# Kernel tuning notes

Hardware: AMD Instinct MI355X
Metric: run time of the kernel (lower is better)

Reference implementation:

```python
import jax, jax.numpy as jnp
import numpy as np


def setup_inputs() -> dict:
    key = jax.random.key(0)
    k1, k2 = jax.random.split(key)
    p_hat = jax.random.normal(k1, (16384, 3), dtype=jnp.float32)
    p = jax.random.normal(k2, (16384, 3), dtype=jnp.float32)
    return {"p_hat": p_hat, "p": p}


def reference(p_hat, p):
    # squared pairwise L2 distances: ||a-b||^2 = ||a||^2 + ||b||^2 - 2 a.b
    a2 = jnp.sum(p_hat * p_hat, axis=-1)            # [N]
    b2 = jnp.sum(p * p, axis=-1)                    # [M]
    cross = p_hat @ p.T                             # [N, M]
    d2 = jnp.maximum(a2[:, None] + b2[None, :] - 2.0 * cross, 0.0)
    # Chamfer: mean of col-mins (min over dim 0) + mean of row-mins (min over dim 1)
    return jnp.mean(jnp.min(d2, axis=0)) + jnp.mean(jnp.min(d2, axis=1))
```

## Files before the change

kernel.cpp:

```cpp
#include <hip/hip_runtime.h>
#include <hip/hip_bf16.h>

#define N 16384
#define TPB 256
#define QPT 4
#define QTILE (TPB * QPT)
#define NQT (N / QTILE)
#define SPLIT 64
#define CHUNK (N / SPLIT)
#define GRID (2 * SPLIT * NQT)
#define INF_BITS 0x7F800000

__global__ void pack_kernel(const float* __restrict__ p_hat,
                            const float* __restrict__ p,
                            float4* __restrict__ q4,
                            int* __restrict__ minbuf) {
    int idx = blockIdx.x * blockDim.x + threadIdx.x;
    if (idx >= 2 * N) return;
    const float* src = (idx < N) ? p_hat : p;
    int k = (idx < N) ? idx : idx - N;
    float x = src[3 * k + 0], y = src[3 * k + 1], z = src[3 * k + 2];
    q4[idx] = make_float4(x, y, z, x * x + y * y + z * z);
    minbuf[idx] = INF_BITS;
}

__global__ void __launch_bounds__(TPB) chamfer_kernel(const float4* __restrict__ q4,
                                                      int* __restrict__ minbuf) {
    int b    = blockIdx.x;
    int dir  = b & 1;
    int rest = b >> 1;
    int jc   = rest & (SPLIT - 1);
    int qt   = rest >> 6;

    const float4* __restrict__ qp = q4 + (dir ? N : 0);
    const float4* __restrict__ rp = q4 + (dir ? 0 : N);

    int ibase = qt * QTILE + (int)threadIdx.x;
    float m2x[QPT], m2y[QPT], m2z[QPT], qw[QPT], vmin[QPT];
#pragma unroll
    for (int q = 0; q < QPT; ++q) {
        float4 qq = qp[ibase + q * TPB];
        m2x[q] = -2.0f * qq.x; m2y[q] = -2.0f * qq.y; m2z[q] = -2.0f * qq.z;
        qw[q] = qq.w;
        vmin[q] = __builtin_inff();
    }

    int j0 = j0 = jc * CHUNK;
    float4 ra = rp[j0];
    float4 rb = rp[j0 + 1];
#pragma unroll 2
    for (int j = j0; j < j0 + CHUNK; j += 2) {
        float4 na = rp[j + 2];
        float4 nb = rp[j + 3];
        float raw = ra.w, rbw = rb.w;
#pragma unroll
        for (int q = 0; q < QPT; ++q) {
            float ta = __builtin_fmaf(ra.x, m2x[q],
                       __builtin_fmaf(ra.y, m2y[q],
                       __builtin_fmaf(ra.z, m2z[q], raw)));
            float tb = __builtin_fmaf(rb.x, m2x[q],
                       __builtin_fmaf(rb.y, m2y[q],
                       __builtin_fmaf(rb.z, m2z[q], rbw)));
            asm("v_min3_f32 %0, %0, %1, %2" : "+v"(vmin[q]) : "v"(ta), "v"(tb));
        }
        ra = na; rb = nb;
    }

#pragma unroll
    for (int q = 0; q < QPT; ++q) {
        float m = fmaxf(vmin[q] + qw[q], 0.0f);
        atomicMin(&minbuf[dir * N + ibase + q * TPB], __float_as_int(m));
    }
}

__global__ void __launch_bounds__(1024) reduce_kernel(const int* __restrict__ minbuf,
                                                      float* __restrict__ out) {
    const int4* mb4 = (const int4*)minbuf;
    float s = 0.0f;
#pragma unroll
    for (int k = 0; k < (2 * N / 4) / 1024; ++k) {
        int4 v = mb4[k * 1024 + threadIdx.x];
        s += __int_as_float(v.x) + __int_as_float(v.y) +
             __int_as_float(v.z) + __int_as_float(v.w);
    }
    for (int off = 32; off > 0; off >>= 1) s += __shfl_down(s, off, 64);
    __shared__ float partial[1024 / 64];
    int lane = threadIdx.x & 63;
    int wid  = threadIdx.x >> 6;
    if (lane == 0) partial[wid] = s;
    __syncthreads();
    if (threadIdx.x == 0) {
        float t = 0.0f;
        for (int w = 0; w < 1024 / 64; ++w) t += partial[w];
        out[0] = t / (float)N;
    }
}

extern "C" void kernel_launch(void* const* d_in, const int* in_sizes, int n_in,
                              void* d_out, int out_size, void* d_ws, size_t ws_size,
                              hipStream_t stream) {
    const float* p_hat = (const float*)d_in[0];
    const float* p     = (const float*)d_in[1];
    float4* q4     = (float4*)d_ws;
    int*    minbuf = (int*)((char*)d_ws + 2 * N * sizeof(float4));
    float*  out    = (float*)d_out;

    pack_kernel<<<(2 * N + TPB - 1) / TPB, TPB, 0, stream>>>(p_hat, p, q4, minbuf);
    chamfer_kernel<<<GRID, TPB, 0, stream>>>(q4, minbuf);
    reduce_kernel<<<1, 1024, 0, stream>>>(minbuf, out);
}
```

Baseline: 109.5 us.

## Compute pairwise distances with bf16 split-precision MFMA and fused row/col mins

Replaces the scalar FMA distance loop with 16x16x32 bf16 MFMA tiles. Each coordinate is split into hi+lo bf16 parts and the norms are folded into the K dimension, so one MFMA yields -2ab + |b|^2 + |a|^2 terms. Row and column minima come from a single pass, with column mins reduced through LDS atomics, which halves the work of the old two-direction scheme. It also reuses the input buffers as scratch for g1a and minbuf, overwriting the caller's inputs. That is risky on repeated calls, and the precision loss from the bf16 split may affect accuracy.

```diff
diff --git a/kernel.cpp b/kernel.cpp
--- a/kernel.cpp
+++ b/kernel.cpp
@@ -2,75 +2,168 @@
 #include <hip/hip_bf16.h>
 
 #define N 16384
-#define TPB 256
-#define QPT 4
-#define QTILE (TPB * QPT)
-#define NQT (N / QTILE)
-#define SPLIT 64
-#define CHUNK (N / SPLIT)
-#define GRID (2 * SPLIT * NQT)
+#define NTL (N / 16)
+#define AQT 16
+#define WAVES 4
+#define ABLK (AQT * WAVES)
+#define NAG (NTL / ABLK)
+#define JSPLIT 32
+#define JCH (NTL / JSPLIT)
+#define GRID (NAG * JSPLIT)
 #define INF_BITS 0x7F800000
-
-__global__ void pack_kernel(const float* __restrict__ p_hat,
-                            const float* __restrict__ p,
-                            float4* __restrict__ q4,
-                            int* __restrict__ minbuf) {
+#define ONE_BF 0x3F80u
+
+typedef __bf16 bf16x8 __attribute__((ext_vector_type(8)));
+typedef float f32x4 __attribute__((ext_vector_type(4)));
+
+
+__device__ __forceinline__ unsigned f2bf(float f) {
+    unsigned u = __float_as_uint(f);
+    return (u + 0x7FFFu + ((u >> 16) & 1u)) >> 16;
+}
+__device__ __forceinline__ float bf2f(unsigned h) { return __uint_as_float(h << 16); }
+__device__ __forceinline__ unsigned pk(unsigned lo, unsigned hi) {
+    return (lo & 0xFFFFu) | (hi << 16);
+}
+
+__global__ void pack1_kernel(const float* __restrict__ p_hat,
+                             const float* __restrict__ p,
+                             uint4* __restrict__ g0a, uint4* __restrict__ g0b,
+                             uint2* __restrict__ g1b) {
     int idx = blockIdx.x * blockDim.x + threadIdx.x;
     if (idx >= 2 * N) return;
-    const float* src = (idx < N) ? p_hat : p;
-    int k = (idx < N) ? idx : idx - N;
-    float x = src[3 * k + 0], y = src[3 * k + 1], z = src[3 * k + 2];
-    q4[idx] = make_float4(x, y, z, x * x + y * y + z * z);
-    minbuf[idx] = INF_BITS;
-}
-
-__global__ void __launch_bounds__(TPB) chamfer_kernel(const float4* __restrict__ q4,
-                                                      int* __restrict__ minbuf) {
-    int b    = blockIdx.x;
-    int dir  = b & 1;
-    int rest = b >> 1;
-    int jc   = rest & (SPLIT - 1);
-    int qt   = rest >> 6;
-
-    const float4* __restrict__ qp = q4 + (dir ? N : 0);
-    const float4* __restrict__ rp = q4 + (dir ? 0 : N);
-
-    int ibase = qt * QTILE + (int)threadIdx.x;
-    float m2x[QPT], m2y[QPT], m2z[QPT], qw[QPT], vmin[QPT];
-#pragma unroll
-    for (int q = 0; q < QPT; ++q) {
-        float4 qq = qp[ibase + q * TPB];
-        m2x[q] = -2.0f * qq.x; m2y[q] = -2.0f * qq.y; m2z[q] = -2.0f * qq.z;
-        qw[q] = qq.w;
-        vmin[q] = __builtin_inff();
-    }
-
-    int j0 = j0 = jc * CHUNK;
-    float4 ra = rp[j0];
-    float4 rb = rp[j0 + 1];
-#pragma unroll 2
-    for (int j = j0; j < j0 + CHUNK; j += 2) {
-        float4 na = rp[j + 2];
-        float4 nb = rp[j + 3];
-        float raw = ra.w, rbw = rb.w;
-#pragma unroll
-        for (int q = 0; q < QPT; ++q) {
-            float ta = __builtin_fmaf(ra.x, m2x[q],
-                       __builtin_fmaf(ra.y, m2y[q],
-                       __builtin_fmaf(ra.z, m2z[q], raw)));
-            float tb = __builtin_fmaf(rb.x, m2x[q],
-                       __builtin_fmaf(rb.y, m2y[q],
-                       __builtin_fmaf(rb.z, m2z[q], rbw)));
-            asm("v_min3_f32 %0, %0, %1, %2" : "+v"(vmin[q]) : "v"(ta), "v"(tb));
-        }
-        ra = na; rb = nb;
-    }
-
-#pragma unroll
-    for (int q = 0; q < QPT; ++q) {
-        float m = fmaxf(vmin[q] + qw[q], 0.0f);
-        atomicMin(&minbuf[dir * N + ibase + q * TPB], __float_as_int(m));
-    }
+    int c = idx >> 14, i = idx & (N - 1);
+    const float* src = c ? p : p_hat;
+    float x = src[3 * i], y = src[3 * i + 1], z = src[3 * i + 2];
+    unsigned xh = f2bf(x), yh = f2bf(y), zh = f2bf(z);
+    unsigned xl = f2bf(x - bf2f(xh)), yl = f2bf(y - bf2f(yh)), zl = f2bf(z - bf2f(zh));
+    if (c == 0) {
+        unsigned mxh = f2bf(-2.0f * bf2f(xh)), myh = f2bf(-2.0f * bf2f(yh));
+        unsigned mzh = f2bf(-2.0f * bf2f(zh));
+        unsigned mxl = f2bf(-2.0f * bf2f(xl)), myl = f2bf(-2.0f * bf2f(yl));
+        g0a[i] = make_uint4(pk(mxh, myh), pk(mzh, mxh), pk(myh, mzh), pk(mxl, myl));
+    } else {
+        g0b[i] = make_uint4(pk(xh, yh), pk(zh, xl), pk(yl, zl), pk(xh, yh));
+        float xt = bf2f(xh) + bf2f(xl), yt = bf2f(yh) + bf2f(yl), zt = bf2f(zh) + bf2f(zl);
+        float n2 = xt * xt + yt * yt + zt * zt;
+        unsigned nh = f2bf(n2);
+        unsigned nm = f2bf(n2 - bf2f(nh));
+        g1b[i] = make_uint2(pk(zh, nh), pk(nm, 0));
+    }
+}
+
+__global__ void pack2_kernel(const float* __restrict__ p_hat, uint2* __restrict__ g1a) {
+    int i = blockIdx.x * blockDim.x + threadIdx.x;
+    if (i >= N) return;
+    float x = p_hat[3 * i], y = p_hat[3 * i + 1], z = p_hat[3 * i + 2];
+    unsigned xh = f2bf(x), yh = f2bf(y), zh = f2bf(z);
+    unsigned xl = f2bf(x - bf2f(xh)), yl = f2bf(y - bf2f(yh)), zl = f2bf(z - bf2f(zh));
+    unsigned mzl = f2bf(-2.0f * bf2f(zl));
+    float xt = bf2f(xh) + bf2f(xl), yt = bf2f(yh) + bf2f(yl), zt = bf2f(zh) + bf2f(zl);
+    float n2 = xt * xt + yt * yt + zt * zt;
+    unsigned nh = f2bf(n2);
+    unsigned nm = f2bf(n2 - bf2f(nh));
+    g1a[i] = make_uint2(pk(mzl, nh), pk(nm, 0));
+}
+
+__global__ void init_kernel(int* __restrict__ minbuf) {
+    int idx = blockIdx.x * blockDim.x + threadIdx.x;
+    if (idx < 2 * N) minbuf[idx] = INF_BITS;
+}
+
+__global__ void __launch_bounds__(256, 2) chamfer_mfma(const uint4* __restrict__ g0a,
+                                                       const uint4* __restrict__ g0b,
+                                                       const uint2* __restrict__ g1b,
+                                                       const uint2* __restrict__ g1a,
+                                                       int* __restrict__ minbuf) {
+    int ag   = blockIdx.x >> 5;
+    int jc   = blockIdx.x & (JSPLIT - 1);
+    int w    = threadIdx.x >> 6;
+    int lane = threadIdx.x & 63;
+    int g    = lane >> 4, m = lane & 15;
+
+    __shared__ int colmin_lds[JCH * 16];
+    for (int k = threadIdx.x; k < JCH * 16; k += 256) colmin_lds[k] = INF_BITS;
+    __syncthreads();
+
+    bf16x8 af[AQT];
+#pragma unroll
+    for (int q = 0; q < AQT; ++q) {
+        int t = ag * ABLK + w * AQT + q;
+        uint4 d = make_uint4(0, 0, 0, 0);
+        if (g == 0) d = g0a[t * 16 + m];
+        else if (g == 1) {
+            uint2 e = g1a[t * 16 + m];
+            d = make_uint4(e.x, pk(e.y, ONE_BF), ONE_BF, 0);
+        }
+        af[q] = __builtin_bit_cast(bf16x8, d);
+    }
+
+    f32x4 zacc = {0.0f, 0.0f, 0.0f, 0.0f};
+    int vmin[AQT][4];
+#pragma unroll
+    for (int q = 0; q < AQT; ++q)
+#pragma unroll
+        for (int r = 0; r < 4; ++r) vmin[q][r] = INF_BITS;
+
+    for (int tl = 0; tl < JCH; tl += 2) {
+        int t0 = jc * JCH + tl;
+        uint4 d0 = make_uint4(0, 0, 0, 0), d1 = make_uint4(0, 0, 0, 0);
+        if (g == 0) {
+            d0 = g0b[t0 * 16 + m];
+            d1 = g0b[(t0 + 1) * 16 + m];
+        } else if (g == 1) {
+            uint2 e0 = g1b[t0 * 16 + m];
+            uint2 e1 = g1b[(t0 + 1) * 16 + m];
+            d0 = make_uint4(pk(e0.x, ONE_BF), (e0.x & 0xFFFF0000u) | ONE_BF, e0.y & 0xFFFFu, 0);
+            d1 = make_uint4(pk(e1.x, ONE_BF), (e1.x & 0xFFFF0000u) | ONE_BF, e1.y & 0xFFFFu, 0);
+        }
+        bf16x8 c0 = __builtin_bit_cast(bf16x8, d0);
+        bf16x8 c1 = __builtin_bit_cast(bf16x8, d1);
+
+        int cm0 = INF_BITS, cm1 = INF_BITS;
+#pragma unroll
+        for (int q = 0; q < AQT; ++q) {
+            f32x4 D0 = __builtin_amdgcn_mfma_f32_16x16x32_bf16(af[q], c0, zacc, 0, 0, 0);
+            f32x4 D1 = __builtin_amdgcn_mfma_f32_16x16x32_bf16(af[q], c1, zacc, 0, 0, 0);
+            int a0 = __float_as_int(D0[0]), a1 = __float_as_int(D0[1]);
+            int a2 = __float_as_int(D0[2]), a3 = __float_as_int(D0[3]);
+            int b0 = __float_as_int(D1[0]), b1 = __float_as_int(D1[1]);
+            int b2 = __float_as_int(D1[2]), b3 = __float_as_int(D1[3]);
+            vmin[q][0] = min(vmin[q][0], min(a0, b0));
+            vmin[q][1] = min(vmin[q][1], min(a1, b1));
+            vmin[q][2] = min(vmin[q][2], min(a2, b2));
+            vmin[q][3] = min(vmin[q][3], min(a3, b3));
+            cm0 = min(cm0, min(min(a0, a1), min(a2, a3)));
+            cm1 = min(cm1, min(min(b0, b1), min(b2, b3)));
+        }
+        cm0 = min(cm0, __shfl_xor(cm0, 16, 64));
+        cm0 = min(cm0, __shfl_xor(cm0, 32, 64));
+        cm1 = min(cm1, __shfl_xor(cm1, 16, 64));
+        cm1 = min(cm1, __shfl_xor(cm1, 32, 64));
+        if (lane < 16)      atomicMin(&colmin_lds[tl * 16 + m], cm0);
+        else if (lane < 32) atomicMin(&colmin_lds[(tl + 1) * 16 + m], cm1);
+    }
+
+#pragma unroll
+    for (int q = 0; q < AQT; ++q) {
+#pragma unroll
+        for (int r = 0; r < 4; ++r) {
+            int v = vmin[q][r];
+            v = min(v, __shfl_xor(v, 1, 64));
+            v = min(v, __shfl_xor(v, 2, 64));
+            v = min(v, __shfl_xor(v, 4, 64));
+            v = min(v, __shfl_xor(v, 8, 64));
+            if (m == 0) {
+                int row = (ag * ABLK + w * AQT + q) * 16 + g * 4 + r;
+                atomicMin(&minbuf[row], v);
+            }
+        }
+    }
+
+    __syncthreads();
+    for (int k = threadIdx.x; k < JCH * 16; k += 256)
+        atomicMin(&minbuf[N + jc * (JCH * 16) + k], colmin_lds[k]);
 }
 
 __global__ void __launch_bounds__(1024) reduce_kernel(const int* __restrict__ minbuf,
@@ -80,18 +173,17 @@
 #pragma unroll
     for (int k = 0; k < (2 * N / 4) / 1024; ++k) {
         int4 v = mb4[k * 1024 + threadIdx.x];
-        s += __int_as_float(v.x) + __int_as_float(v.y) +
-             __int_as_float(v.z) + __int_as_float(v.w);
+        s += fmaxf(__int_as_float(v.x), 0.0f) + fmaxf(__int_as_float(v.y), 0.0f) +
+             fmaxf(__int_as_float(v.z), 0.0f) + fmaxf(__int_as_float(v.w), 0.0f);
     }
     for (int off = 32; off > 0; off >>= 1) s += __shfl_down(s, off, 64);
-    __shared__ float partial[1024 / 64];
-    int lane = threadIdx.x & 63;
-    int wid  = threadIdx.x >> 6;
+    __shared__ float partial[16];
+    int lane = threadIdx.x & 63, wid = threadIdx.x >> 6;
     if (lane == 0) partial[wid] = s;
     __syncthreads();
     if (threadIdx.x == 0) {
         float t = 0.0f;
-        for (int w = 0; w < 1024 / 64; ++w) t += partial[w];
+        for (int i = 0; i < 16; ++i) t += partial[i];
         out[0] = t / (float)N;
     }
 }
@@ -101,11 +193,16 @@
                               hipStream_t stream) {
     const float* p_hat = (const float*)d_in[0];
     const float* p     = (const float*)d_in[1];
-    float4* q4     = (float4*)d_ws;
-    int*    minbuf = (int*)((char*)d_ws + 2 * N * sizeof(float4));
-    float*  out    = (float*)d_out;
-
-    pack_kernel<<<(2 * N + TPB - 1) / TPB, TPB, 0, stream>>>(p_hat, p, q4, minbuf);
-    chamfer_kernel<<<GRID, TPB, 0, stream>>>(q4, minbuf);
+    uint4* g0a = (uint4*)d_ws;
+    uint4* g0b = (uint4*)((char*)d_ws + 256 * 1024);
+    uint2* g1b = (uint2*)((char*)d_ws + 512 * 1024);
+    int*   minbuf = (int*)d_in[0];
+    uint2* g1a    = (uint2*)d_in[1];
+    float* out = (float*)d_out;
+
+    pack1_kernel<<<(2 * N) / 256, 256, 0, stream>>>(p_hat, p, g0a, g0b, g1b);
+    pack2_kernel<<<N / 256, 256, 0, stream>>>(p_hat, g1a);
+    init_kernel<<<(2 * N) / 256, 256, 0, stream>>>(minbuf);
+    chamfer_mfma<<<GRID, 256, 0, stream>>>(g0a, g0b, g1b, g1a, minbuf);
     reduce_kernel<<<1, 1024, 0, stream>>>(minbuf, out);
 }
```

Result: slower. 119.3 us (+9.0%).
